# Kernel optimization log

Hardware: AMD Instinct MI355X
Metric: run time of the kernel (lower is better)

The kernel has to match this reference:

```python
import jax, jax.numpy as jnp
import numpy as np
import math

NUM_GROUPS = 32
EPS = 1e-5


def setup_inputs() -> dict:
    key = jax.random.key(0)
    k1, k2, k3 = jax.random.split(key, 3)
    B, C, H, W = 8, 128, 64, 64
    x = jax.random.normal(k1, (B, C, H, W), dtype=jnp.float32)
    gn_w = jnp.ones((C,), dtype=jnp.float32)
    gn_b = jnp.zeros((C,), dtype=jnp.float32)
    # 1x1 conv -> dense weight [3C, C] (kernel dims squeezed)
    qkv_w = jax.random.normal(k2, (3 * C, C), dtype=jnp.float32) * (1.0 / math.sqrt(C))
    qkv_b = jax.random.normal(k3, (3 * C,), dtype=jnp.float32) * 0.01
    return {"x": x, "gn_w": gn_w, "gn_b": gn_b, "qkv_w": qkv_w, "qkv_b": qkv_b}


def _group_norm(x, w, b):
    B, C, H, W = x.shape
    xg = x.reshape(B, NUM_GROUPS, C // NUM_GROUPS, H, W)
    mean = xg.mean(axis=(2, 3, 4), keepdims=True)
    var = xg.var(axis=(2, 3, 4), keepdims=True)
    xn = ((xg - mean) * jax.lax.rsqrt(var + EPS)).reshape(B, C, H, W)
    return xn * w[None, :, None, None] + b[None, :, None, None]


def reference(x, gn_w, gn_b, qkv_w, qkv_b):
    B, C, H, W = x.shape
    scale = 1.0 / math.sqrt(C)
    h = _group_norm(x, gn_w, gn_b)
    # 1x1 conv == channel-mixing matmul: [B, 3C, H*W]
    hf = h.reshape(B, C, H * W)
    qkv = jnp.einsum('oc,bcs->bos', qkv_w, hf) + qkv_b[None, :, None]
    q, k, v = jnp.split(qkv, 3, axis=1)  # each [B, C, S]
    attn = jnp.einsum('bct,bcs->bts', q, k) * scale  # [B, S, S]
    attn = jax.nn.softmax(attn, axis=2)
    a = jnp.einsum('bts,bcs->bct', attn, v)  # [B, C, S]
    return x * a.reshape(B, C, H, W)
```

## Files before the change

### kernel.cpp

```cpp
#include <hip/hip_runtime.h>
#include <hip/hip_bf16.h>
#include <stdint.h>

typedef unsigned short u16;
typedef unsigned int   u32;
typedef __attribute__((ext_vector_type(8)))  short bf16x8;
typedef __attribute__((ext_vector_type(8)))  unsigned short u16x8;
typedef __attribute__((ext_vector_type(4)))  float f32x4;
typedef __attribute__((ext_vector_type(16))) float f32x16;

#define SC2 0.1275174475f

#define MFMA3216(A, B, C) __builtin_amdgcn_mfma_f32_32x32x16_bf16(A, B, C, 0, 0, 0)
#define MFMA1632(A, B, C) __builtin_amdgcn_mfma_f32_16x16x32_bf16(A, B, C, 0, 0, 0)

__device__ __forceinline__ float bf2f(u16 u) {
    union { u32 i; float f; } t; t.i = ((u32)u) << 16; return t.f;
}
__device__ __forceinline__ u16 f2bf(float f) {
    union { u32 i; float f; } t; t.f = f;
    u32 b = t.i;
    return (u16)((b + 0x7fffu + ((b >> 16) & 1u)) >> 16);
}
__device__ __forceinline__ u32 packbf(float a, float b) {
    union { __hip_bfloat162 h; u32 u; } c;
    c.h = __float22bfloat162_rn(float2{a, b});
    return c.u;
}

__device__ __forceinline__ void gload16(const u16* g, u16* l) {
    __builtin_amdgcn_global_load_lds(
        (const __attribute__((address_space(1))) void*)g,
        (__attribute__((address_space(3))) void*)l, 16, 0, 0);
}

__global__ __launch_bounds__(256) void stats_kernel(
    const float* __restrict__ x, const float* __restrict__ gw,
    const float* __restrict__ gb, float* __restrict__ gp, float* __restrict__ bp)
{
    int b = blockIdx.x & 7, g = blockIdx.x >> 3;
    long base = ((long)(b * 128 + g * 4)) << 12;
    const float4* x4 = (const float4*)(x + base);

    float s = 0.f, ss = 0.f;
    for (int i = threadIdx.x; i < 4096; i += 256) {
        float4 v = x4[i];
        s  += v.x + v.y + v.z + v.w;
        ss += v.x * v.x + v.y * v.y + v.z * v.z + v.w * v.w;
    }
    #pragma unroll
    for (int off = 32; off > 0; off >>= 1) {
        s  += __shfl_xor(s,  off);
        ss += __shfl_xor(ss, off);
    }
    __shared__ float red[8];
    int wid = threadIdx.x >> 6;
    if ((threadIdx.x & 63) == 0) { red[wid * 2] = s; red[wid * 2 + 1] = ss; }
    __syncthreads();
    s  = red[0] + red[2] + red[4] + red[6];
    ss = red[1] + red[3] + red[5] + red[7];

    float mean = s * (1.f / 16384.f);
    float var  = ss * (1.f / 16384.f) - mean * mean;
    float rs   = rsqrtf(var + 1e-5f);

    if (threadIdx.x < 4) {
        int c = g * 4 + threadIdx.x;
        float gamma = gw[c] * rs;
        gp[b * 128 + c] = gamma;
        bp[b * 128 + c] = gb[c] - mean * gamma;
    }
}

__global__ __launch_bounds__(256) void wconv_kernel(
    const float* __restrict__ w, u16* __restrict__ wbf)
{
    int idx = (blockIdx.x * 256 + threadIdx.x) * 4;
    float4 v = *(const float4*)&w[idx];
    ushort4 o = { f2bf(v.x), f2bf(v.y), f2bf(v.z), f2bf(v.w) };
    *(ushort4*)&wbf[idx] = o;
}

__global__ __launch_bounds__(256) void apply_kernel(
    const float* __restrict__ x, const float* __restrict__ gp,
    const float* __restrict__ bp, u16* __restrict__ hn)
{
    __shared__ u16 ldsT[128 * 128];
    __shared__ float gpl[128], bpl[128];
    int b = blockIdx.x & 7, st = blockIdx.x >> 3;
    int s0 = st << 7;
    int t = threadIdx.x;
    if (t < 128) { gpl[t] = gp[b * 128 + t]; bpl[t] = bp[b * 128 + t]; }
    __syncthreads();

    const float* xb = x + ((long)b << 19);
    int sl = t & 127, chalf = t >> 7;
    #pragma unroll
    for (int c8 = 0; c8 < 8; ++c8) {
        int CH = chalf * 8 + c8;
        u16 tmp[8];
        #pragma unroll
        for (int j = 0; j < 8; ++j) {
            int c = CH * 8 + j;
            float v = xb[((long)c << 12) + s0 + sl];
            tmp[j] = f2bf(v * gpl[c] + bpl[c]);
        }
        *(u16x8*)&ldsT[sl * 128 + ((CH ^ (sl & 15)) << 3)] = *(u16x8*)tmp;
    }
    __syncthreads();

    u16* hnb = hn + ((long)b << 19);
    int s = t >> 1, h = t & 1;
    #pragma unroll
    for (int i = 0; i < 8; ++i) {
        int CH = h * 8 + i;
        u16x8 v = *(u16x8*)&ldsT[s * 128 + ((CH ^ (s & 15)) << 3)];
        *(u16x8*)&hnb[(long)(s0 + s) * 128 + CH * 8] = v;
    }
}

__global__ __launch_bounds__(256) void qkvm_kernel(
    const u16* __restrict__ hn, const u16* __restrict__ wbf,
    const float* __restrict__ bias,
    u16* __restrict__ Qt, u16* __restrict__ Kt, u16* __restrict__ Vv)
{
    __shared__ u16 ldsH[64 * 128];
    int tid = threadIdx.x, lane = tid & 63, wv = tid >> 6;
    int g = lane >> 4, t = lane & 15;
    int b = blockIdx.x & 7, stile = blockIdx.x >> 3;
    int s0 = stile << 6;

    const u16* hnb = hn + ((long)b << 19);
    #pragma unroll
    for (int i = 0; i < 4; ++i) {
        int seg = wv * 4 + i;
        int n = seg * 64 + lane;
        int s = n >> 4, SL = n & 15;
        int gch = SL ^ (s & 15);
        gload16(hnb + (long)(s0 + s) * 128 + gch * 8, &ldsH[seg * 512]);
    }
    __syncthreads();

    bf16x8 hf[4];
    int slq = (wv << 4) + t;
    #pragma unroll
    for (int ks = 0; ks < 4; ++ks)
        hf[ks] = *(const bf16x8*)&ldsH[slq * 128 + ((((ks << 2) + g) ^ t) << 3)];

    u16* Qtb = Qt + ((long)b << 19);
    u16* Ktb = Kt + ((long)b << 19);
    u16* Vb  = Vv + ((long)b << 19);
    int srow = s0 + (wv << 4) + (g << 2);

    #pragma unroll
    for (int ot = 0; ot < 8; ++ot) {
        bf16x8 wf[4];
        #pragma unroll
        for (int ks = 0; ks < 4; ++ks)
            wf[ks] = *(const bf16x8*)&wbf[(ot * 16 + t) * 128 + ks * 32 + g * 8];
        float bv = bias[ot * 16 + t];
        f32x4 acc = (f32x4){bv, bv, bv, bv};
        #pragma unroll
        for (int ks = 0; ks < 4; ++ks)
            acc = MFMA1632(hf[ks], wf[ks], acc);
        #pragma unroll
        for (int r = 0; r < 4; ++r)
            Qtb[(long)(srow + r) * 128 + ot * 16 + t] = f2bf(acc[r]);
    }
    #pragma unroll
    for (int ot = 8; ot < 16; ++ot) {
        bf16x8 wf[4];
        #pragma unroll
        for (int ks = 0; ks < 4; ++ks)
            wf[ks] = *(const bf16x8*)&wbf[(ot * 16 + t) * 128 + ks * 32 + g * 8];
        float bv = bias[ot * 16 + t];
        f32x4 acc = (f32x4){bv, bv, bv, bv};
        #pragma unroll
        for (int ks = 0; ks < 4; ++ks)
            acc = MFMA1632(hf[ks], wf[ks], acc);
        #pragma unroll
        for (int r = 0; r < 4; ++r)
            Ktb[(long)(srow + r) * 128 + (ot - 8) * 16 + t] = f2bf(acc[r]);
    }
    #pragma unroll
    for (int ot = 16; ot < 24; ++ot) {
        bf16x8 wf[4];
        #pragma unroll
        for (int ks = 0; ks < 4; ++ks)
            wf[ks] = *(const bf16x8*)&wbf[(ot * 16 + t) * 128 + ks * 32 + g * 8];
        float4 b4 = *(const float4*)&bias[ot * 16 + (g << 2)];
        f32x4 acc = (f32x4){b4.x, b4.y, b4.z, b4.w};
        #pragma unroll
        for (int ks = 0; ks < 4; ++ks)
            acc = MFMA1632(wf[ks], hf[ks], acc);
        #pragma unroll
        for (int r = 0; r < 4; ++r) {
            int cv = (ot - 16) * 16 + (g << 2) + r;
            Vb[((long)cv << 12) + s0 + (wv << 4) + t] = f2bf(acc[r]);
        }
    }
}

__global__ __launch_bounds__(256) void attn_kernel(
    const u16* __restrict__ Qt, const u16* __restrict__ Kt,
    const u16* __restrict__ Vv, const float* __restrict__ x,
    float* __restrict__ out)
{
    __shared__ u16 ldsK[2][8192];
    __shared__ u16 ldsV[2][8192];
    __shared__ float mls[2][2][2][32];

    int tid = threadIdx.x, lane = tid & 63, wv = tid >> 6;
    int wq = wv >> 1, wk = wv & 1;
    int q5 = lane & 31, h = lane >> 5;
    int b = blockIdx.x & 7, qb = blockIdx.x >> 3;
    int s0 = qb << 6;

    const u16* Qb = Qt + ((long)b << 19);
    const u16* Kb = Kt + ((long)b << 19);
    const u16* Vb = Vv + ((long)b << 19);

    bf16x8 qf[8];
    {
        long qrow = (long)(s0 + (wq << 5) + q5) << 7;
        #pragma unroll
        for (int d = 0; d < 8; ++d)
            qf[d] = *(const bf16x8*)&Qb[qrow + (d << 4) + (h << 3)];
    }

    f32x16 acco[4];
    #pragma unroll
    for (int cb = 0; cb < 4; ++cb)
        #pragma unroll
        for (int r = 0; r < 16; ++r) acco[cb][r] = 0.f;
    float m = -3e38f, llp = 0.f;

    u32 kso[4], vso[4];
    #pragma unroll
    for (int i = 0; i < 4; ++i) {
        int idx = (((wv << 2) + i) << 6) + lane;
        int s = idx >> 4, ch = idx & 15;
        kso[i] = s * 128 + ((ch ^ (s & 7)) << 3);
        int c = idx >> 3, c8 = idx & 7;
        vso[i] = c * 4096 + ((c8 ^ (c & 7)) << 3);
    }

    int sKey = (wk << 5) + q5;
    u32 kfo[8];
    #pragma unroll
    for (int d = 0; d < 8; ++d) {
        int ch = (d << 1) + h;
        kfo[d] = sKey * 128 + ((ch ^ (sKey & 7)) << 3);
    }
    u32 vfo[8];
    #pragma unroll
    for (int cb = 0; cb < 4; ++cb)
        #pragma unroll
        for (int ks = 0; ks < 2; ++ks) {
            int c = (cb << 5) + q5;
            int ch8 = (wk << 2) + (ks << 1) + h;
            vfo[cb * 2 + ks] = c * 64 + ((ch8 ^ (c & 7)) << 3);
        }

    auto STAGE = [&](int buf) {
        #pragma unroll
        for (int i = 0; i < 4; ++i) {
            int seg = (wv << 2) + i;
            gload16(Kb + kso[i], &ldsK[buf][seg << 9]);
            gload16(Vb + vso[i], &ldsV[buf][seg << 9]);
            kso[i] += 8192;
            vso[i] += 64;
        }
    };

    STAGE(0);
    __syncthreads();
    int cur = 0;

    for (int kt = 0; kt < 64; ++kt) {
        if (kt < 63) STAGE(cur ^ 1);

        const u16* lK = ldsK[cur];
        const u16* lV = ldsV[cur];

        bf16x8 kf[8];
        #pragma unroll
        for (int d = 0; d < 8; ++d)
            kf[d] = *(const bf16x8*)&lK[kfo[d]];

        f32x16 s;
        #pragma unroll
        for (int r = 0; r < 16; ++r) s[r] = 0.f;
        __builtin_amdgcn_s_setprio(1);
        #pragma unroll
        for (int d = 0; d < 8; ++d)
            s = MFMA3216(kf[d], qf[d], s);
        __builtin_amdgcn_s_setprio(0);

        float px = s[0];
        #pragma unroll
        for (int r = 1; r < 16; ++r) px = fmaxf(px, s[r]);
        px = fmaxf(px, __shfl_xor(px, 32));
        px *= SC2;
        if (!__all(px - m <= 12.0f)) {
            float mn = fmaxf(m, px);
            float al = exp2f(m - mn);
            llp *= al;
            #pragma unroll
            for (int cb = 0; cb < 4; ++cb)
                #pragma unroll
                for (int r = 0; r < 16; ++r) acco[cb][r] *= al;
            m = mn;
        }
        float e[16];
        float psum = 0.f;
        #pragma unroll
        for (int r = 0; r < 16; ++r) {
            e[r] = exp2f(fmaf(s[r], SC2, -m));
            psum += e[r];
        }
        llp += psum;

        u32 pk0[2], pk1[2], pk2[2], pk3[2];
        pk0[0] = packbf(e[0],  e[1]);  pk0[1] = packbf(e[2],  e[3]);
        pk1[0] = packbf(e[4],  e[5]);  pk1[1] = packbf(e[6],  e[7]);
        pk2[0] = packbf(e[8],  e[9]);  pk2[1] = packbf(e[10], e[11]);
        pk3[0] = packbf(e[12], e[13]); pk3[1] = packbf(e[14], e[15]);
        u32 t0[2], t1[2];
        #pragma unroll
        for (int j = 0; j < 2; ++j) {
            t0[j] = (u32)__shfl_xor((int)(h ? pk0[j] : pk1[j]), 32);
            t1[j] = (u32)__shfl_xor((int)(h ? pk2[j] : pk3[j]), 32);
        }
        union { u32 u[4]; bf16x8 v; } pb0, pb1;
        pb0.u[0] = h ? t0[0]  : pk0[0];
        pb0.u[1] = h ? t0[1]  : pk0[1];
        pb0.u[2] = h ? pk1[0] : t0[0];
        pb0.u[3] = h ? pk1[1] : t0[1];
        pb1.u[0] = h ? t1[0]  : pk2[0];
        pb1.u[1] = h ? t1[1]  : pk2[1];
        pb1.u[2] = h ? pk3[0] : t1[0];
        pb1.u[3] = h ? pk3[1] : t1[1];

        __builtin_amdgcn_s_setprio(1);
        #pragma unroll
        for (int cb = 0; cb < 4; ++cb) {
            bf16x8 v0 = *(const bf16x8*)&lV[vfo[cb * 2 + 0]];
            acco[cb] = MFMA3216(v0, pb0.v, acco[cb]);
            bf16x8 v1 = *(const bf16x8*)&lV[vfo[cb * 2 + 1]];
            acco[cb] = MFMA3216(v1, pb1.v, acco[cb]);
        }
        __builtin_amdgcn_s_setprio(0);

        __syncthreads();
        cur ^= 1;
    }

    float ll = llp + __shfl_xor(llp, 32);
    if (h == 0) { mls[wq][wk][0][q5] = m; mls[wq][wk][1][q5] = ll; }
    __syncthreads();
    float mo = mls[wq][wk ^ 1][0][q5], lo = mls[wq][wk ^ 1][1][q5];
    float mf = fmaxf(m, mo);
    float lf = ll * exp2f(m - mf) + lo * exp2f(mo - mf);
    float sc = exp2f(m - mf) / lf;

    float* mrg = (wk == 0) ? (float*)&ldsK[0][0] : (float*)&ldsV[0][0];
    #pragma unroll
    for (int cb = 0; cb < 4; ++cb)
        #pragma unroll
        for (int r = 0; r < 16; ++r) {
            int c = (cb << 5) + (r & 3) + ((r >> 2) << 3) + (h << 2);
            mrg[(c << 6) + (wq << 5) + q5] = acco[cb][r] * sc;
        }
    __syncthreads();

    const float* mA = (const float*)&ldsK[0][0];
    const float* mB = (const float*)&ldsV[0][0];
    const float* xb = x + ((long)b << 19);
    float* ob = out + ((long)b << 19);
    int q6 = tid & 63, c0 = tid >> 6;
    #pragma unroll 8
    for (int i = 0; i < 32; ++i) {
        int c = (i << 2) + c0;
        float v = mA[(c << 6) + q6] + mB[(c << 6) + q6];
        long gi = ((long)c << 12) + s0 + q6;
        ob[gi] = xb[gi] * v;
    }
}

extern "C" void kernel_launch(void* const* d_in, const int* in_sizes, int n_in,
                              void* d_out, int out_size, void* d_ws, size_t ws_size,
                              hipStream_t stream)
{
    const float* x    = (const float*)d_in[0];
    const float* gw   = (const float*)d_in[1];
    const float* gb   = (const float*)d_in[2];
    const float* w    = (const float*)d_in[3];
    const float* bias = (const float*)d_in[4];
    float* out = (float*)d_out;

    u16* hn  = (u16*)d_ws;
    u16* Qt  = hn + (size_t)8 * 4096 * 128;
    u16* Kt  = Qt + (size_t)8 * 4096 * 128;
    u16* Vv  = Kt + (size_t)8 * 4096 * 128;
    u16* wbf = Vv + (size_t)8 * 128 * 4096;
    float* gp = (float*)(wbf + (size_t)384 * 128);
    float* bp = gp + 1024;

    stats_kernel<<<256, 256, 0, stream>>>(x, gw, gb, gp, bp);
    wconv_kernel<<<48, 256, 0, stream>>>(w, wbf);
    apply_kernel<<<256, 256, 0, stream>>>(x, gp, bp, hn);
    qkvm_kernel<<<512, 256, 0, stream>>>(hn, wbf, bias, Qt, Kt, Vv);
    attn_kernel<<<512, 256, 0, stream>>>(Qt, Kt, Vv, x, out);
}
```

Baseline: 158.6 us.

## Split attention key range across four waves per query tile, single-buffer LDS

Doubles the attention block to 512 threads so each 32-query half is handled by four waves, each covering a quarter of every 128-key tile. The loop drops from 64 to 32 tiles and from double-buffered to single-buffered LDS, with a sync after each load, so load latency is no longer overlapped with compute. A four-way max/sum merge and a two-pass LDS reduction combine the partial outputs. The max and sum reductions are also rewritten as trees.

After: 353.1 us. 2.23x slower.

```diff
diff --git a/kernel.cpp b/kernel.cpp
--- a/kernel.cpp
+++ b/kernel.cpp
@@ -201,17 +201,19 @@
     }
 }
 
-__global__ __launch_bounds__(256) void attn_kernel(
+__global__ __launch_bounds__(512, 4) void attn_kernel(
     const u16* __restrict__ Qt, const u16* __restrict__ Kt,
     const u16* __restrict__ Vv, const float* __restrict__ x,
     float* __restrict__ out)
 {
-    __shared__ u16 ldsK[2][8192];
-    __shared__ u16 ldsV[2][8192];
-    __shared__ float mls[2][2][2][32];
+    __shared__ u16 ldsBuf[32768];
+    __shared__ float mls[2][4][2][32];
+
+    u16* ldsK = ldsBuf;
+    u16* ldsV = ldsBuf + 16384;
 
     int tid = threadIdx.x, lane = tid & 63, wv = tid >> 6;
-    int wq = wv >> 1, wk = wv & 1;
+    int wq = wv >> 2, wk = wv & 3;
     int q5 = lane & 31, h = lane >> 5;
     int b = blockIdx.x & 7, qb = blockIdx.x >> 3;
     int s0 = qb << 6;
@@ -238,11 +240,10 @@
     u32 kso[4], vso[4];
     #pragma unroll
     for (int i = 0; i < 4; ++i) {
-        int idx = (((wv << 2) + i) << 6) + lane;
-        int s = idx >> 4, ch = idx & 15;
-        kso[i] = s * 128 + ((ch ^ (s & 7)) << 3);
-        int c = idx >> 3, c8 = idx & 7;
-        vso[i] = c * 4096 + ((c8 ^ (c & 7)) << 3);
+        int n = (((wv << 2) + i) << 6) + lane;
+        int key = n >> 4, ch = n & 15;
+        kso[i] = key * 128 + ((ch ^ (key & 7)) << 3);
+        vso[i] = key * 4096 + ((ch ^ (key & 7)) << 3);
     }
 
     int sKey = (wk << 5) + q5;
@@ -258,35 +259,25 @@
         #pragma unroll
         for (int ks = 0; ks < 2; ++ks) {
             int c = (cb << 5) + q5;
-            int ch8 = (wk << 2) + (ks << 1) + h;
-            vfo[cb * 2 + ks] = c * 64 + ((ch8 ^ (c & 7)) << 3);
-        }
-
-    auto STAGE = [&](int buf) {
+            int g8 = (wk << 2) + (ks << 1) + h;
+            vfo[cb * 2 + ks] = c * 128 + ((g8 ^ (c & 7)) << 3);
+        }
+
+    for (int kt = 0; kt < 32; ++kt) {
         #pragma unroll
         for (int i = 0; i < 4; ++i) {
             int seg = (wv << 2) + i;
-            gload16(Kb + kso[i], &ldsK[buf][seg << 9]);
-            gload16(Vb + vso[i], &ldsV[buf][seg << 9]);
-            kso[i] += 8192;
-            vso[i] += 64;
-        }
-    };
-
-    STAGE(0);
-    __syncthreads();
-    int cur = 0;
-
-    for (int kt = 0; kt < 64; ++kt) {
-        if (kt < 63) STAGE(cur ^ 1);
-
-        const u16* lK = ldsK[cur];
-        const u16* lV = ldsV[cur];
+            gload16(Kb + kso[i], &ldsK[seg << 9]);
+            gload16(Vb + vso[i], &ldsV[seg << 9]);
+            kso[i] += 16384;
+            vso[i] += 128;
+        }
+        __syncthreads();
 
         bf16x8 kf[8];
         #pragma unroll
         for (int d = 0; d < 8; ++d)
-            kf[d] = *(const bf16x8*)&lK[kfo[d]];
+            kf[d] = *(const bf16x8*)&ldsK[kfo[d]];
 
         f32x16 s;
         #pragma unroll
@@ -297,9 +288,12 @@
             s = MFMA3216(kf[d], qf[d], s);
         __builtin_amdgcn_s_setprio(0);
 
-        float px = s[0];
-        #pragma unroll
-        for (int r = 1; r < 16; ++r) px = fmaxf(px, s[r]);
+        float x0 = fmaxf(s[0], s[1]),  x1 = fmaxf(s[2], s[3]);
+        float x2 = fmaxf(s[4], s[5]),  x3 = fmaxf(s[6], s[7]);
+        float x4 = fmaxf(s[8], s[9]),  x5 = fmaxf(s[10], s[11]);
+        float x6 = fmaxf(s[12], s[13]), x7 = fmaxf(s[14], s[15]);
+        float px = fmaxf(fmaxf(fmaxf(x0, x1), fmaxf(x2, x3)),
+                         fmaxf(fmaxf(x4, x5), fmaxf(x6, x7)));
         px = fmaxf(px, __shfl_xor(px, 32));
         px *= SC2;
         if (!__all(px - m <= 12.0f)) {
@@ -313,13 +307,14 @@
             m = mn;
         }
         float e[16];
-        float psum = 0.f;
-        #pragma unroll
-        for (int r = 0; r < 16; ++r) {
+        #pragma unroll
+        for (int r = 0; r < 16; ++r)
             e[r] = exp2f(fmaf(s[r], SC2, -m));
-            psum += e[r];
-        }
-        llp += psum;
+        float s0a = (e[0] + e[1]) + (e[2] + e[3]);
+        float s1a = (e[4] + e[5]) + (e[6] + e[7]);
+        float s2a = (e[8] + e[9]) + (e[10] + e[11]);
+        float s3a = (e[12] + e[13]) + (e[14] + e[15]);
+        llp += (s0a + s1a) + (s2a + s3a);
 
         u32 pk0[2], pk1[2], pk2[2], pk3[2];
         pk0[0] = packbf(e[0],  e[1]);  pk0[1] = packbf(e[2],  e[3]);
@@ -345,46 +340,56 @@
         __builtin_amdgcn_s_setprio(1);
         #pragma unroll
         for (int cb = 0; cb < 4; ++cb) {
-            bf16x8 v0 = *(const bf16x8*)&lV[vfo[cb * 2 + 0]];
+            bf16x8 v0 = *(const bf16x8*)&ldsV[vfo[cb * 2 + 0]];
             acco[cb] = MFMA3216(v0, pb0.v, acco[cb]);
-            bf16x8 v1 = *(const bf16x8*)&lV[vfo[cb * 2 + 1]];
+            bf16x8 v1 = *(const bf16x8*)&ldsV[vfo[cb * 2 + 1]];
             acco[cb] = MFMA3216(v1, pb1.v, acco[cb]);
         }
         __builtin_amdgcn_s_setprio(0);
 
         __syncthreads();
-        cur ^= 1;
     }
 
     float ll = llp + __shfl_xor(llp, 32);
     if (h == 0) { mls[wq][wk][0][q5] = m; mls[wq][wk][1][q5] = ll; }
     __syncthreads();
-    float mo = mls[wq][wk ^ 1][0][q5], lo = mls[wq][wk ^ 1][1][q5];
-    float mf = fmaxf(m, mo);
-    float lf = ll * exp2f(m - mf) + lo * exp2f(mo - mf);
+    float m0 = mls[wq][0][0][q5], l0 = mls[wq][0][1][q5];
+    float m1 = mls[wq][1][0][q5], l1 = mls[wq][1][1][q5];
+    float m2 = mls[wq][2][0][q5], l2 = mls[wq][2][1][q5];
+    float m3 = mls[wq][3][0][q5], l3 = mls[wq][3][1][q5];
+    float mf = fmaxf(fmaxf(m0, m1), fmaxf(m2, m3));
+    float lf = l0 * exp2f(m0 - mf) + l1 * exp2f(m1 - mf)
+             + l2 * exp2f(m2 - mf) + l3 * exp2f(m3 - mf);
     float sc = exp2f(m - mf) / lf;
 
-    float* mrg = (wk == 0) ? (float*)&ldsK[0][0] : (float*)&ldsV[0][0];
-    #pragma unroll
-    for (int cb = 0; cb < 4; ++cb)
-        #pragma unroll
-        for (int r = 0; r < 16; ++r) {
-            int c = (cb << 5) + (r & 3) + ((r >> 2) << 3) + (h << 2);
-            mrg[(c << 6) + (wq << 5) + q5] = acco[cb][r] * sc;
-        }
-    __syncthreads();
-
-    const float* mA = (const float*)&ldsK[0][0];
-    const float* mB = (const float*)&ldsV[0][0];
+    float* mrg = (float*)ldsBuf;
     const float* xb = x + ((long)b << 19);
     float* ob = out + ((long)b << 19);
-    int q6 = tid & 63, c0 = tid >> 6;
-    #pragma unroll 8
-    for (int i = 0; i < 32; ++i) {
-        int c = (i << 2) + c0;
-        float v = mA[(c << 6) + q6] + mB[(c << 6) + q6];
-        long gi = ((long)c << 12) + s0 + q6;
-        ob[gi] = xb[gi] * v;
+    int rg = ((wk << 1) + wq) << 11;
+
+    #pragma unroll
+    for (int p = 0; p < 2; ++p) {
+        #pragma unroll
+        for (int cb2 = 0; cb2 < 2; ++cb2) {
+            int cb = (p << 1) + cb2;
+            #pragma unroll
+            for (int r = 0; r < 16; ++r) {
+                int cl = (cb2 << 5) + (r & 3) + ((r >> 2) << 3) + (h << 2);
+                mrg[rg + (cl << 5) + q5] = acco[cb][r] * sc;
+            }
+        }
+        __syncthreads();
+        #pragma unroll
+        for (int j = 0; j < 8; ++j) {
+            int idx = (j << 9) + tid;
+            int cl = idx >> 6, q = idx & 63;
+            int wqr = q >> 5, ql = q & 31;
+            int o = (wqr << 11) + (cl << 5) + ql;
+            float sum = (mrg[o] + mrg[o + 4096]) + (mrg[o + 8192] + mrg[o + 12288]);
+            long gi = (((long)((p << 6) + cl)) << 12) + s0 + q;
+            ob[gi] = xb[gi] * sum;
+        }
+        if (p == 0) __syncthreads();
     }
 }
 
@@ -411,5 +416,5 @@
     wconv_kernel<<<48, 256, 0, stream>>>(w, wbf);
     apply_kernel<<<256, 256, 0, stream>>>(x, gp, bp, hn);
     qkvm_kernel<<<512, 256, 0, stream>>>(hn, wbf, bias, Qt, Kt, Vv);
-    attn_kernel<<<512, 256, 0, stream>>>(Qt, Kt, Vv, x, out);
-}
+    attn_kernel<<<512, 512, 0, stream>>>(Qt, Kt, Vv, x, out);
+}
```
